# Kernel optimization log

Hardware: AMD Instinct MI355X
Metric: run time of the kernel (lower is better)

Reference implementation:

```python
import jax, jax.numpy as jnp
import numpy as np

BATCH, SEQ, IN, HID, OUT = 4096, 512, 2, 128, 1


def setup_inputs() -> dict:
    key = jax.random.key(0)
    k_x, k_wih, k_bih, k_who, k_bho = jax.random.split(key, 5)
    s = 1.0 / np.sqrt(IN + HID)
    return {
        "x": jax.random.normal(k_x, (BATCH, SEQ, IN), dtype=jnp.float32),
        "W_ih": jax.random.normal(k_wih, (HID, IN + HID), dtype=jnp.float32) * s,
        "b_ih": jax.random.normal(k_bih, (HID,), dtype=jnp.float32) * s,
        "W_ho": jax.random.normal(k_who, (OUT, HID), dtype=jnp.float32) / np.sqrt(HID),
        "b_bho" if False else "b_ho": jax.random.normal(k_bho, (OUT,), dtype=jnp.float32) / np.sqrt(HID),
    }


def reference(x, W_ih, b_ih, W_ho, b_ho):
    # x: [B, T, I]. Elman cell: h = tanh([x_t, h] @ W_ih^T + b_ih)
    B = x.shape[0]
    h0 = jnp.zeros((B, W_ih.shape[0]), dtype=x.dtype)
    # split W_ih into input and hidden blocks (equivalent to concat+matmul)
    W_x = W_ih[:, : x.shape[-1]]   # [H, I]
    W_h = W_ih[:, x.shape[-1] :]   # [H, H]

    def step(h, x_t):
        h_new = jnp.tanh(x_t @ W_x.T + h @ W_h.T + b_ih)
        return h_new, None

    xs = jnp.swapaxes(x, 0, 1)  # [T, B, I] for scan over time
    h_final, _ = jax.lax.scan(step, h0, xs)
    return h_final @ W_ho.T + b_ho  # [B, OUT]
```

## Files before the change

### kernel.cpp

```cpp
#include <hip/hip_runtime.h>


constexpr int BATCH   = 4096;
constexpr int SEQ     = 512;
constexpr int INP     = 2;
constexpr int HID     = 128;
constexpr int BM      = 16;
constexpr int THREADS = 512;

typedef short bf16x8 __attribute__((ext_vector_type(8)));
typedef float f32x4  __attribute__((ext_vector_type(4)));

__device__ inline unsigned short f2bf(float f) {
    unsigned u = __float_as_uint(f);
    return (unsigned short)((u + 0x7FFFu + ((u >> 16) & 1u)) >> 16);
}
__device__ inline float bf2f(unsigned short s) {
    return __uint_as_float(((unsigned)s) << 16);
}
__device__ inline unsigned cvt_pk_bf16(float a, float b) {
    unsigned r;
    asm("v_cvt_pk_bf16_f32 %0, %1, %2" : "=v"(r) : "v"(a), "v"(b));
    return r;
}
__device__ inline void lds_barrier() {
    asm volatile("s_waitcnt lgkmcnt(0)\n\ts_barrier" ::: "memory");
}

__global__ __launch_bounds__(THREADS, 2)
void elman_mfma11(const float* __restrict__ x,
                  const float* __restrict__ W_ih,
                  const float* __restrict__ b_ih,
                  const float* __restrict__ W_ho,
                  const float* __restrict__ b_ho,
                  float* __restrict__ out)
{
    __shared__ unsigned short hlds[2][2][BM][HID];
    __shared__ float red[BM][8];

    const int tid  = threadIdx.x;
    const int lane = tid & 63;
    const int w    = tid >> 6;
    const int l15  = lane & 15;
    const int g    = lane >> 4;
    const int B0   = blockIdx.x * BM;

    bf16x8 whi[4], wlo[4];
    {
        const float* Wrow = W_ih + (size_t)(w * 16 + l15) * (INP + HID) + INP;
        #pragma unroll
        for (int kt = 0; kt < 4; ++kt) {
            const int k0 = kt * 32 + g * 8;
            #pragma unroll
            for (int i = 0; i < 8; ++i) {
                const float wv = Wrow[k0 + i];
                const unsigned short hi = f2bf(wv);
                whi[kt][i] = (short)hi;
                wlo[kt][i] = (short)f2bf(wv - bf2f(hi));
            }
        }
    }

    float wx0v[4], wx1v[4], bjv[4], whov[4];
    #pragma unroll
    for (int reg = 0; reg < 4; ++reg) {
        const int jj = w * 16 + g * 4 + reg;
        const float* Wr = W_ih + (size_t)jj * (INP + HID);
        wx0v[reg] = Wr[0];
        wx1v[reg] = Wr[1];
        bjv[reg]  = b_ih[jj];
        whov[reg] = W_ho[jj];
    }

    int roff[4];
    #pragma unroll
    for (int kt = 0; kt < 4; ++kt)
        roff[kt] = l15 * 256 + ((kt * 64 + g * 16) ^ (l15 << 4));
    const int woff = l15 * 256 + (((w * 32 + (g & 2) * 8)) ^ (l15 << 4)) + (g & 1) * 8;

    reinterpret_cast<float4*>(hlds)[tid]       = float4{0.f, 0.f, 0.f, 0.f};
    reinterpret_cast<float4*>(hlds)[tid + 512] = float4{0.f, 0.f, 0.f, 0.f};

    const float* xrow = x + (size_t)(B0 + l15) * (SEQ * INP);
    float2 xv0 = *reinterpret_cast<const float2*>(xrow);
    float2 xv1 = *reinterpret_cast<const float2*>(xrow + INP);

    __syncthreads();

    char* hbA = (char*)&hlds[0][0][0][0];
    char* lbA = (char*)&hlds[0][1][0][0];
    char* hbB = (char*)&hlds[1][0][0][0];
    char* lbB = (char*)&hlds[1][1][0][0];

    float hv[4] = {0.f, 0.f, 0.f, 0.f};

#define RNN_STEP(HP, LP, HN, LN, XV)                                           \
    {                                                                          \
        bf16x8 ahi[4], alo[4];                                                 \
        _Pragma("unroll")                                                      \
        for (int kt = 0; kt < 4; ++kt) {                                       \
            ahi[kt] = *reinterpret_cast<const bf16x8*>((HP) + roff[kt]);       \
            alo[kt] = *reinterpret_cast<const bf16x8*>((LP) + roff[kt]);       \
        }                                                                      \
        f32x4 a0 = {0.f, 0.f, 0.f, 0.f};                                       \
        f32x4 a1 = {0.f, 0.f, 0.f, 0.f};                                       \
        f32x4 a2 = {0.f, 0.f, 0.f, 0.f};                                       \
        _Pragma("unroll")                                                      \
        for (int kt = 0; kt < 4; ++kt) {                                       \
            a0 = __builtin_amdgcn_mfma_f32_16x16x32_bf16(whi[kt], ahi[kt], a0, 0, 0, 0); \
            a1 = __builtin_amdgcn_mfma_f32_16x16x32_bf16(whi[kt], alo[kt], a1, 0, 0, 0); \
            a2 = __builtin_amdgcn_mfma_f32_16x16x32_bf16(wlo[kt], ahi[kt], a2, 0, 0, 0); \
        }                                                                      \
        const float2 xv = (XV);                                                \
        float hcur[4];                                                         \
        _Pragma("unroll")                                                      \
        for (int reg = 0; reg < 4; ++reg) {                                    \
            const float acc = (a0[reg] + a1[reg] + a2[reg])                    \
                            + fmaf(wx0v[reg], xv.x, fmaf(wx1v[reg], xv.y, bjv[reg])); \
            const float e = __expf(acc + acc);                                 \
            hcur[reg] = 1.0f - __fdividef(2.0f, e + 1.0f);      \
            hv[reg]   = hcur[reg];                                             \
        }                                                                      \
        const unsigned c01 = cvt_pk_bf16(hcur[0], hcur[1]);                    \
        const unsigned c23 = cvt_pk_bf16(hcur[2], hcur[3]);                    \
        const float h0b = __uint_as_float(c01 << 16);                          \
        const float h1b = __uint_as_float(c01 & 0xFFFF0000u);                  \
        const float h2b = __uint_as_float(c23 << 16);                          \
        const float h3b = __uint_as_float(c23 & 0xFFFF0000u);                  \
        const unsigned l01 = cvt_pk_bf16(hcur[0] - h0b, hcur[1] - h1b);        \
        const unsigned l23 = cvt_pk_bf16(hcur[2] - h2b, hcur[3] - h3b);        \
        *reinterpret_cast<uint2*>((HN) + woff) = uint2{c01, c23};              \
        *reinterpret_cast<uint2*>((LN) + woff) = uint2{l01, l23};              \
        lds_barrier();                                                         \
    }

    #pragma unroll 1
    for (int t2 = 0; t2 < SEQ; t2 += 2) {
        const int tn = (t2 + 2 < SEQ) ? (t2 + 2) : 0;
        const float2 xn0 = *reinterpret_cast<const float2*>(xrow + (size_t)tn * INP);
        const float2 xn1 = *reinterpret_cast<const float2*>(xrow + (size_t)tn * INP + INP);

        RNN_STEP(hbA, lbA, hbB, lbB, xv0)
        RNN_STEP(hbB, lbB, hbA, lbA, xv1)

        xv0 = xn0;
        xv1 = xn1;
    }
#undef RNN_STEP

    float part = 0.f;
    #pragma unroll
    for (int reg = 0; reg < 4; ++reg) part = fmaf(whov[reg], hv[reg], part);
    part += __shfl_xor(part, 16);
    part += __shfl_xor(part, 32);
    if (lane < 16) red[l15][w] = part;
    __syncthreads();
    if (tid < BM) {
        float s = b_ho[0];
        #pragma unroll
        for (int q = 0; q < 8; ++q) s += red[tid][q];
        out[B0 + tid] = s;
    }
}

extern "C" void kernel_launch(void* const* d_in, const int* in_sizes, int n_in,
                              void* d_out, int out_size, void* d_ws, size_t ws_size,
                              hipStream_t stream)
{
    (void)in_sizes; (void)n_in; (void)out_size; (void)d_ws; (void)ws_size;
    const float* x    = (const float*)d_in[0];
    const float* W_ih = (const float*)d_in[1];
    const float* b_ih = (const float*)d_in[2];
    const float* W_ho = (const float*)d_in[3];
    const float* b_ho = (const float*)d_in[4];
    float* out = (float*)d_out;

    dim3 grid(BATCH / BM);
    dim3 block(THREADS);
    elman_mfma11<<<grid, block, 0, stream>>>(x, W_ih, b_ih, W_ho, b_ho, out);
}
```

Before: 302.5 us.

## Halve block to 4 waves, each computing two 16-row hidden chunks

Each block now uses 256 threads instead of 512, and every wave computes 32 hidden units (two MFMA row tiles) rather than 16. Each A-fragment read from LDS is reused for two sets of MFMAs, so per-step LDS reads per block drop, and the per-step barrier synchronises half as many waves. In exchange each wave carries twice the weight registers and a longer serial MFMA chain per step, and launch bounds drop to one block, which may lower occupancy and latency hiding across the 256 blocks.

```diff
diff --git a/kernel.cpp b/kernel.cpp
--- a/kernel.cpp
+++ b/kernel.cpp
@@ -6,7 +6,7 @@
 constexpr int INP     = 2;
 constexpr int HID     = 128;
 constexpr int BM      = 16;
-constexpr int THREADS = 512;
+constexpr int THREADS = 256;
 
 typedef short bf16x8 __attribute__((ext_vector_type(8)));
 typedef float f32x4  __attribute__((ext_vector_type(4)));
@@ -27,8 +27,8 @@
     asm volatile("s_waitcnt lgkmcnt(0)\n\ts_barrier" ::: "memory");
 }
 
-__global__ __launch_bounds__(THREADS, 2)
-void elman_mfma11(const float* __restrict__ x,
+__global__ __launch_bounds__(THREADS, 1)
+void elman_mfma12(const float* __restrict__ x,
                   const float* __restrict__ W_ih,
                   const float* __restrict__ b_ih,
                   const float* __restrict__ W_ho,
@@ -36,7 +36,7 @@
                   float* __restrict__ out)
 {
     __shared__ unsigned short hlds[2][2][BM][HID];
-    __shared__ float red[BM][8];
+    __shared__ float red[BM][4];
 
     const int tid  = threadIdx.x;
     const int lane = tid & 63;
@@ -45,9 +45,10 @@
     const int g    = lane >> 4;
     const int B0   = blockIdx.x * BM;
 
-    bf16x8 whi[4], wlo[4];
-    {
-        const float* Wrow = W_ih + (size_t)(w * 16 + l15) * (INP + HID) + INP;
+    bf16x8 whi[2][4], wlo[2][4];
+    #pragma unroll
+    for (int c = 0; c < 2; ++c) {
+        const float* Wrow = W_ih + (size_t)(w * 32 + c * 16 + l15) * (INP + HID) + INP;
         #pragma unroll
         for (int kt = 0; kt < 4; ++kt) {
             const int k0 = kt * 32 + g * 8;
@@ -55,31 +56,37 @@
             for (int i = 0; i < 8; ++i) {
                 const float wv = Wrow[k0 + i];
                 const unsigned short hi = f2bf(wv);
-                whi[kt][i] = (short)hi;
-                wlo[kt][i] = (short)f2bf(wv - bf2f(hi));
+                whi[c][kt][i] = (short)hi;
+                wlo[c][kt][i] = (short)f2bf(wv - bf2f(hi));
             }
         }
     }
 
-    float wx0v[4], wx1v[4], bjv[4], whov[4];
-    #pragma unroll
-    for (int reg = 0; reg < 4; ++reg) {
-        const int jj = w * 16 + g * 4 + reg;
-        const float* Wr = W_ih + (size_t)jj * (INP + HID);
-        wx0v[reg] = Wr[0];
-        wx1v[reg] = Wr[1];
-        bjv[reg]  = b_ih[jj];
-        whov[reg] = W_ho[jj];
-    }
+    float wx0v[2][4], wx1v[2][4], bjv[2][4], whov[2][4];
+    #pragma unroll
+    for (int c = 0; c < 2; ++c)
+        #pragma unroll
+        for (int reg = 0; reg < 4; ++reg) {
+            const int jj = w * 32 + c * 16 + g * 4 + reg;
+            const float* Wr = W_ih + (size_t)jj * (INP + HID);
+            wx0v[c][reg] = Wr[0];
+            wx1v[c][reg] = Wr[1];
+            bjv[c][reg]  = b_ih[jj];
+            whov[c][reg] = W_ho[jj];
+        }
 
     int roff[4];
     #pragma unroll
     for (int kt = 0; kt < 4; ++kt)
         roff[kt] = l15 * 256 + ((kt * 64 + g * 16) ^ (l15 << 4));
-    const int woff = l15 * 256 + (((w * 32 + (g & 2) * 8)) ^ (l15 << 4)) + (g & 1) * 8;
-
-    reinterpret_cast<float4*>(hlds)[tid]       = float4{0.f, 0.f, 0.f, 0.f};
-    reinterpret_cast<float4*>(hlds)[tid + 512] = float4{0.f, 0.f, 0.f, 0.f};
+    int woff[2];
+    #pragma unroll
+    for (int c = 0; c < 2; ++c)
+        woff[c] = l15 * 256 + ((w * 64 + c * 32 + (g & 2) * 8) ^ (l15 << 4)) + (g & 1) * 8;
+
+    #pragma unroll
+    for (int q = 0; q < 4; ++q)
+        reinterpret_cast<float4*>(hlds)[tid + 256 * q] = float4{0.f, 0.f, 0.f, 0.f};
 
     const float* xrow = x + (size_t)(B0 + l15) * (SEQ * INP);
     float2 xv0 = *reinterpret_cast<const float2*>(xrow);
@@ -92,7 +99,11 @@
     char* hbB = (char*)&hlds[1][0][0][0];
     char* lbB = (char*)&hlds[1][1][0][0];
 
-    float hv[4] = {0.f, 0.f, 0.f, 0.f};
+    float hv[2][4];
+    #pragma unroll
+    for (int c = 0; c < 2; ++c)
+        #pragma unroll
+        for (int reg = 0; reg < 4; ++reg) hv[c][reg] = 0.f;
 
 #define RNN_STEP(HP, LP, HN, LN, XV)                                           \
     {                                                                          \
@@ -102,35 +113,46 @@
             ahi[kt] = *reinterpret_cast<const bf16x8*>((HP) + roff[kt]);       \
             alo[kt] = *reinterpret_cast<const bf16x8*>((LP) + roff[kt]);       \
         }                                                                      \
-        f32x4 a0 = {0.f, 0.f, 0.f, 0.f};                                       \
-        f32x4 a1 = {0.f, 0.f, 0.f, 0.f};                                       \
-        f32x4 a2 = {0.f, 0.f, 0.f, 0.f};                                       \
+        f32x4 a0[2], a1[2], a2[2];                                             \
+        _Pragma("unroll")                                                      \
+        for (int c = 0; c < 2; ++c) {                                          \
+            a0[c] = f32x4{0.f, 0.f, 0.f, 0.f};                                 \
+            a1[c] = f32x4{0.f, 0.f, 0.f, 0.f};                                 \
+            a2[c] = f32x4{0.f, 0.f, 0.f, 0.f};                                 \
+        }                                                                      \
         _Pragma("unroll")                                                      \
         for (int kt = 0; kt < 4; ++kt) {                                       \
-            a0 = __builtin_amdgcn_mfma_f32_16x16x32_bf16(whi[kt], ahi[kt], a0, 0, 0, 0); \
-            a1 = __builtin_amdgcn_mfma_f32_16x16x32_bf16(whi[kt], alo[kt], a1, 0, 0, 0); \
-            a2 = __builtin_amdgcn_mfma_f32_16x16x32_bf16(wlo[kt], ahi[kt], a2, 0, 0, 0); \
+            a0[0] = __builtin_amdgcn_mfma_f32_16x16x32_bf16(whi[0][kt], ahi[kt], a0[0], 0, 0, 0); \
+            a1[0] = __builtin_amdgcn_mfma_f32_16x16x32_bf16(whi[0][kt], alo[kt], a1[0], 0, 0, 0); \
+            a2[0] = __builtin_amdgcn_mfma_f32_16x16x32_bf16(wlo[0][kt], ahi[kt], a2[0], 0, 0, 0); \
+            a0[1] = __builtin_amdgcn_mfma_f32_16x16x32_bf16(whi[1][kt], ahi[kt], a0[1], 0, 0, 0); \
+            a1[1] = __builtin_amdgcn_mfma_f32_16x16x32_bf16(whi[1][kt], alo[kt], a1[1], 0, 0, 0); \
+            a2[1] = __builtin_amdgcn_mfma_f32_16x16x32_bf16(wlo[1][kt], ahi[kt], a2[1], 0, 0, 0); \
         }                                                                      \
         const float2 xv = (XV);                                                \
-        float hcur[4];                                                         \
-        _Pragma("unroll")                                                      \
-        for (int reg = 0; reg < 4; ++reg) {                                    \
-            const float acc = (a0[reg] + a1[reg] + a2[reg])                    \
-                            + fmaf(wx0v[reg], xv.x, fmaf(wx1v[reg], xv.y, bjv[reg])); \
-            const float e = __expf(acc + acc);                                 \
-            hcur[reg] = 1.0f - __fdividef(2.0f, e + 1.0f);      \
-            hv[reg]   = hcur[reg];                                             \
-        }                                                                      \
-        const unsigned c01 = cvt_pk_bf16(hcur[0], hcur[1]);                    \
-        const unsigned c23 = cvt_pk_bf16(hcur[2], hcur[3]);                    \
-        const float h0b = __uint_as_float(c01 << 16);                          \
-        const float h1b = __uint_as_float(c01 & 0xFFFF0000u);                  \
-        const float h2b = __uint_as_float(c23 << 16);                          \
-        const float h3b = __uint_as_float(c23 & 0xFFFF0000u);                  \
-        const unsigned l01 = cvt_pk_bf16(hcur[0] - h0b, hcur[1] - h1b);        \
-        const unsigned l23 = cvt_pk_bf16(hcur[2] - h2b, hcur[3] - h3b);        \
-        *reinterpret_cast<uint2*>((HN) + woff) = uint2{c01, c23};              \
-        *reinterpret_cast<uint2*>((LN) + woff) = uint2{l01, l23};              \
+        _Pragma("unroll")                                                      \
+        for (int c = 0; c < 2; ++c) {                                          \
+            float hcur[4];                                                     \
+            _Pragma("unroll")                                                  \
+            for (int reg = 0; reg < 4; ++reg) {                                \
+                const float acc = (a0[c][reg] + a1[c][reg] + a2[c][reg])       \
+                                + fmaf(wx0v[c][reg], xv.x,                     \
+                                  fmaf(wx1v[c][reg], xv.y, bjv[c][reg]));      \
+                const float e = __expf(acc + acc);                             \
+                hcur[reg] = 1.0f - __fdividef(2.0f, e + 1.0f);       \
+                hv[c][reg] = hcur[reg];                                        \
+            }                                                                  \
+            const unsigned c01 = cvt_pk_bf16(hcur[0], hcur[1]);                \
+            const unsigned c23 = cvt_pk_bf16(hcur[2], hcur[3]);                \
+            const float h0b = __uint_as_float(c01 << 16);                      \
+            const float h1b = __uint_as_float(c01 & 0xFFFF0000u);              \
+            const float h2b = __uint_as_float(c23 << 16);                      \
+            const float h3b = __uint_as_float(c23 & 0xFFFF0000u);              \
+            const unsigned l01 = cvt_pk_bf16(hcur[0] - h0b, hcur[1] - h1b);    \
+            const unsigned l23 = cvt_pk_bf16(hcur[2] - h2b, hcur[3] - h3b);    \
+            *reinterpret_cast<uint2*>((HN) + woff[c]) = uint2{c01, c23};       \
+            *reinterpret_cast<uint2*>((LN) + woff[c]) = uint2{l01, l23};       \
+        }                                                                      \
         lds_barrier();                                                         \
     }
 
@@ -150,7 +172,10 @@
 
     float part = 0.f;
     #pragma unroll
-    for (int reg = 0; reg < 4; ++reg) part = fmaf(whov[reg], hv[reg], part);
+    for (int c = 0; c < 2; ++c)
+        #pragma unroll
+        for (int reg = 0; reg < 4; ++reg)
+            part = fmaf(whov[c][reg], hv[c][reg], part);
     part += __shfl_xor(part, 16);
     part += __shfl_xor(part, 32);
     if (lane < 16) red[l15][w] = part;
@@ -158,7 +183,7 @@
     if (tid < BM) {
         float s = b_ho[0];
         #pragma unroll
-        for (int q = 0; q < 8; ++q) s += red[tid][q];
+        for (int q = 0; q < 4; ++q) s += red[tid][q];
         out[B0 + tid] = s;
     }
 }
@@ -177,5 +202,5 @@
 
     dim3 grid(BATCH / BM);
     dim3 block(THREADS);
-    elman_mfma11<<<grid, block, 0, stream>>>(x, W_ih, b_ih, W_ho, b_ho, out);
-}
+    elman_mfma12<<<grid, block, 0, stream>>>(x, W_ih, b_ih, W_ho, b_ho, out);
+}
```

After: 390.6 us. +29.1%, slower.
